# Optimization experiments

Hardware: AMD Instinct MI355X
Metric: run time of the kernel (lower is better)

The kernel has to match this reference:

```python
import jax, jax.numpy as jnp
import numpy as np

HID = 64      # hidden_dim
HEADS = 4     # attention heads
CH = HID // HEADS  # 16 per-head channels
EDIM = 6      # edge_dim
NEG = 0.2     # leaky_relu negative slope


def _glorot(key, shape):
    fan_in, fan_out = shape[0], shape[-1]
    s = np.sqrt(6.0 / (fan_in + fan_out)).astype(np.float32)
    return jax.random.uniform(key, shape, jnp.float32, -s, s)


def setup_inputs() -> dict:
    key = jax.random.key(0)
    ks = iter(jax.random.split(key, 48))
    N, E, T = 100000, 1200000, 20000
    inp = {
        "x": jax.random.normal(next(ks), (N, 7), jnp.float32),
        "pos": jax.random.normal(next(ks), (N, 3), jnp.float32),
        "node_type": jax.random.randint(next(ks), (N,), 0, 2),
        "edge_index": jax.random.randint(next(ks), (2, E), 0, N),
        "edge_attr": jax.random.normal(next(ks), (E, EDIM), jnp.float32),
        "num_tracks": T,
        "hidden_state": jax.random.normal(next(ks), (T, HID), jnp.float32),
        # params
        "type_emb": jax.random.normal(next(ks), (2, 8), jnp.float32),
        "enc_W1": _glorot(next(ks), (18, HID)), "enc_b1": jnp.zeros((HID,), jnp.float32),
        "enc_W2": _glorot(next(ks), (HID, HID)), "enc_b2": jnp.zeros((HID,), jnp.float32),
        "gru_Wi": _glorot(next(ks), (HID, 3 * HID)), "gru_bi": jnp.zeros((3 * HID,), jnp.float32),
        "gru_Wh": _glorot(next(ks), (HID, 3 * HID)), "gru_bh": jnp.zeros((3 * HID,), jnp.float32),
        "dec_W1": _glorot(next(ks), (HID, HID)), "dec_b1": jnp.zeros((HID,), jnp.float32),
        "dec_W2": _glorot(next(ks), (HID, 7)), "dec_b2": jnp.zeros((7,), jnp.float32),
    }
    for g in ("g1", "g2"):
        inp[g + "_Wl"] = _glorot(next(ks), (HID, HID))
        inp[g + "_bl"] = jnp.zeros((HID,), jnp.float32)
        inp[g + "_Wr"] = _glorot(next(ks), (HID, HID))
        inp[g + "_br"] = jnp.zeros((HID,), jnp.float32)
        inp[g + "_We"] = _glorot(next(ks), (EDIM, HID))
        inp[g + "_att"] = _glorot(next(ks), (HEADS, CH))
        inp[g + "_bias"] = jnp.zeros((HID,), jnp.float32)
    return inp


def _segment_softmax(e, seg, n):
    m = jax.ops.segment_max(e, seg, num_segments=n)
    m = jnp.where(jnp.isfinite(m), m, 0.0)
    ex = jnp.exp(e - m[seg])
    s = jax.ops.segment_sum(ex, seg, num_segments=n)
    return ex / (s[seg] + 1e-16)


def _gatv2(h, src, dst, eattr, Wl, bl, Wr, br, We, att, bias):
    N = h.shape[0]
    xl = (h @ Wl + bl).reshape(N, HEADS, CH)
    xr = (h @ Wr + br).reshape(N, HEADS, CH)
    ea = (eattr @ We).reshape(-1, HEADS, CH)
    g = jax.nn.leaky_relu(xl[src] + xr[dst] + ea, NEG)      # [E, H, C]
    e = jnp.einsum('ehc,hc->eh', g, att)                     # [E, H]
    alpha = _segment_softmax(e, dst, N)                      # [E, H]
    msg = xl[src] * alpha[..., None]                         # [E, H, C]
    out = jax.ops.segment_sum(msg, dst, num_segments=N)
    return out.reshape(N, HID) + bias, alpha


def reference(x, pos, node_type, edge_index, edge_attr, num_tracks, hidden_state,
              type_emb, enc_W1, enc_b1, enc_W2, enc_b2,
              g1_Wl, g1_bl, g1_Wr, g1_br, g1_We, g1_att, g1_bias,
              g2_Wl, g2_bl, g2_Wr, g2_br, g2_We, g2_att, g2_bias,
              gru_Wi, gru_bi, gru_Wh, gru_bh,
              dec_W1, dec_b1, dec_W2, dec_b2):
    N = x.shape[0]
    h = jnp.concatenate([x, pos, type_emb[node_type]], axis=-1)
    h = jax.nn.relu(h @ enc_W1 + enc_b1) @ enc_W2 + enc_b2

    # PyG GATv2Conv: add self loops, edge_attr fill_value='mean' (mean of incoming edges)
    src, dst = edge_index[0], edge_index[1]
    deg = jax.ops.segment_sum(jnp.ones(src.shape[0], jnp.float32), dst, num_segments=N)
    loop_attr = jax.ops.segment_sum(edge_attr, dst, num_segments=N) / jnp.maximum(deg, 1.0)[:, None]
    ar = jnp.arange(N)
    src_a = jnp.concatenate([src, ar])
    dst_a = jnp.concatenate([dst, ar])
    eattr_a = jnp.concatenate([edge_attr, loop_attr], axis=0)

    h1, a1 = _gatv2(h, src_a, dst_a, eattr_a, g1_Wl, g1_bl, g1_Wr, g1_br, g1_We, g1_att, g1_bias)
    h1 = jax.nn.relu(h1)
    h2, a2 = _gatv2(h1, src_a, dst_a, eattr_a, g2_Wl, g2_bl, g2_Wr, g2_br, g2_We, g2_att, g2_bias)

    # GRUCell on the first num_tracks nodes
    ht = h2[:num_tracks]
    gi = ht @ gru_Wi + gru_bi
    gh = hidden_state @ gru_Wh + gru_bh
    r = jax.nn.sigmoid(gi[:, :HID] + gh[:, :HID])
    z = jax.nn.sigmoid(gi[:, HID:2 * HID] + gh[:, HID:2 * HID])
    n = jnp.tanh(gi[:, 2 * HID:] + r * gh[:, 2 * HID:])
    new_tracks = (1.0 - z) * n + z * hidden_state

    new_full = jnp.concatenate([new_tracks, h2[num_tracks:]], axis=0)
    out = jax.nn.relu(new_full @ dec_W1 + dec_b1) @ dec_W2 + dec_b2  # [N, 7]
    final = out.at[:, :3].set(pos + out[:, :3])
    final = final.at[:, 3:6].set(x[:, :3] + out[:, 3:6])
    return final, new_full, a1, a2
```

## Files before the change

### kernel.cpp

```cpp
#include <hip/hip_runtime.h>

#define NEG 0.2f
#define LOG2E 1.44269504088896f
typedef unsigned short u16;

__device__ __forceinline__ float sigmoidf_(float v){ return 1.f/(1.f+__expf(-v)); }
__device__ __forceinline__ int rfl_(int v){ return __builtin_amdgcn_readfirstlane(v); }
__device__ __forceinline__ float bf2f_(unsigned u){ return __uint_as_float(u<<16); }
__device__ __forceinline__ u16 f2bf_(float f){
  unsigned u = __float_as_uint(f);
  u += 0x7FFFu + ((u>>16)&1u);
  return (u16)(u>>16);
}
template<int C>
__device__ __forceinline__ float dppadd_(float p){
  int r = __builtin_amdgcn_update_dpp(0, __float_as_int(p), C, 0xF, 0xF, true);
  return p + __int_as_float(r);
}
__device__ __forceinline__ float dppsum16_(float p){
  p = dppadd_<0x121>(p);
  p = dppadd_<0x122>(p);
  p = dppadd_<0x124>(p);
  p = dppadd_<0x128>(p);
  return p;
}

__global__ __launch_bounds__(256) void encdeg_kernel(
    const float* __restrict__ x, const float* __restrict__ pos,
    const int* __restrict__ ntype, const float* __restrict__ temb,
    const float* __restrict__ W1, const float* __restrict__ b1,
    const float* __restrict__ W2, const float* __restrict__ b2,
    float* __restrict__ hout,
    const int* __restrict__ ei, int* __restrict__ deg,
    int encB, int E, int N)
{
  __shared__ float sW1[18*64];
  __shared__ float sW2[4096];
  __shared__ float fT[4][8*20];
  __shared__ float tT[4][8*64];
  if ((int)blockIdx.x >= encB){
    int base = ((int)blockIdx.x - encB)*1024 + (int)threadIdx.x;
    #pragma unroll
    for (int j=0;j<4;j++){
      int e = base + j*256;
      if (e < E) atomicAdd(deg + ei[E+e], 1);
    }
    return;
  }
  for (int i=threadIdx.x; i<18*64; i+=256) sW1[i]=W1[i];
  for (int i=threadIdx.x; i<4096; i+=256)  sW2[i]=W2[i];
  __syncthreads();
  int lane = threadIdx.x & 63;
  int wid  = threadIdx.x >> 6;
  int n0 = (blockIdx.x*4 + wid)*8;
  if (n0 >= N) return;
  float b1v=b1[lane], b2v=b2[lane];
  #pragma unroll
  for (int m=0;m<8;m++){
    int n=n0+m; float fv=0.f;
    if (n<N){
      if (lane<7)       fv=x[(size_t)n*7+lane];
      else if (lane<10) fv=pos[(size_t)n*3+lane-7];
      else if (lane<18) fv=temb[ntype[n]*8+lane-10];
    }
    if (lane<20) fT[wid][m*20+lane]=fv;
  }
  float t[8];
  #pragma unroll
  for (int m=0;m<8;m++) t[m]=b1v;
  #pragma unroll 2
  for (int k=0;k<18;k++){
    float w=sW1[k*64+lane];
    #pragma unroll
    for (int m=0;m<8;m++) t[m] += fT[wid][m*20+k]*w;
  }
  #pragma unroll
  for (int m=0;m<8;m++){ t[m]=fmaxf(t[m],0.f); tT[wid][m*64+lane]=t[m]; }
  float o[8];
  #pragma unroll
  for (int m=0;m<8;m++) o[m]=b2v;
  #pragma unroll 2
  for (int k=0;k<64;k++){
    float w=sW2[k*64+lane];
    #pragma unroll
    for (int m=0;m<8;m++) o[m] += tT[wid][m*64+k]*w;
  }
  #pragma unroll
  for (int m=0;m<8;m++){ int n=n0+m; if (n<N) hout[(size_t)n*64+lane]=o[m]; }
}

__global__ __launch_bounds__(256) void alloc_kernel(
    const int* __restrict__ deg, int* __restrict__ offs, int* __restrict__ cursor,
    int* __restrict__ counter, int N)
{
  __shared__ int wsum[4], woff[4], sbase;
  int lane = threadIdx.x & 63, w = threadIdx.x >> 6;
  int base = blockIdx.x*1024 + threadIdx.x*4;
  int v[4]; int s=0;
  #pragma unroll
  for (int j=0;j<4;j++){ int i=base+j; v[j]=(i<N)?deg[i]:0; s+=v[j]; }
  int inc=s;
  #pragma unroll
  for (int d=1;d<64;d<<=1){ int t=__shfl_up(inc,d); if (lane>=d) inc+=t; }
  if (lane==63) wsum[w]=inc;
  __syncthreads();
  if (threadIdx.x==0){
    woff[0]=0; woff[1]=wsum[0]; woff[2]=wsum[0]+wsum[1]; woff[3]=wsum[0]+wsum[1]+wsum[2];
    sbase = atomicAdd(counter, woff[3]+wsum[3]);
  }
  __syncthreads();
  int excl = sbase + woff[w] + (inc - s);
  #pragma unroll
  for (int j=0;j<4;j++){
    int i=base+j;
    if (i<N){ offs[i]=excl; cursor[i]=excl; }
    excl+=v[j];
  }
}

__global__ __launch_bounds__(256) void xfrmfill_kernel(
    const float* __restrict__ hin,
    const float* __restrict__ Wl, const float* __restrict__ bl,
    const float* __restrict__ Wr, const float* __restrict__ br,
    u16* __restrict__ xlo, u16* __restrict__ xro,
    const int* __restrict__ ei, const float* __restrict__ eattr,
    int* __restrict__ cursor, float4* __restrict__ slots,
    int xfB, int E, int N)
{
  __shared__ float hT[4][16*64];
  if ((int)blockIdx.x >= xfB){
    int base = ((int)blockIdx.x - xfB)*1024 + (int)threadIdx.x;
    #pragma unroll
    for (int j=0;j<4;j++){
      int e = base + j*256;
      if (e < E){
        int dst = ei[E + e];
        unsigned slot = (unsigned)atomicAdd(cursor + dst, 1);
        const float2* ep = (const float2*)(eattr + (size_t)e*6);
        float2 p0=ep[0], p1=ep[1], p2=ep[2];
        float4 a, b;
        a.x = __int_as_float(e); a.y = __int_as_float(ei[e]);
        a.z = p0.x; a.w = p0.y;
        b.x = p1.x; b.y = p1.y; b.z = p2.x; b.w = p2.y;
        slots[slot*2u]   = a;
        slots[slot*2u+1] = b;
      }
    }
    return;
  }
  int lane=threadIdx.x&63;
  int wid=threadIdx.x>>6;
  int n0=(blockIdx.x*4+wid)*16;
  if (n0>=N) return;
  #pragma unroll
  for (int m=0;m<16;m++){
    int n=n0+m;
    hT[wid][m*64+lane] = (n<N)? hin[(size_t)n*64+lane] : 0.f;
  }
  float blv=bl[lane], brv=br[lane];
  float al[16], ar[16];
  #pragma unroll
  for (int m=0;m<16;m++){ al[m]=blv; ar[m]=brv; }
  #pragma unroll 2
  for (int k=0;k<64;k++){
    float wl=Wl[k*64+lane], wr=Wr[k*64+lane];
    #pragma unroll
    for (int m=0;m<16;m++){
      float hb = hT[wid][m*64+k];
      al[m]+=hb*wl; ar[m]+=hb*wr;
    }
  }
  #pragma unroll
  for (int m=0;m<16;m++){
    int n=n0+m;
    if (n<N){ xlo[(((unsigned)n)<<6)+lane]=f2bf_(al[m]); xro[(((unsigned)n)<<6)+lane]=f2bf_(ar[m]); }
  }
}

__global__ __launch_bounds__(256) void xfrm_kernel(
    const float* __restrict__ hin,
    const float* __restrict__ Wl, const float* __restrict__ bl,
    const float* __restrict__ Wr, const float* __restrict__ br,
    u16* __restrict__ xlo, u16* __restrict__ xro, int N)
{
  __shared__ float sWl[4096], sWr[4096];
  __shared__ float hT[4][16*64];
  for (int i=threadIdx.x;i<4096;i+=256){ sWl[i]=Wl[i]; sWr[i]=Wr[i]; }
  __syncthreads();
  int lane=threadIdx.x&63;
  int wid=threadIdx.x>>6;
  int n0=(blockIdx.x*4+wid)*16;
  if (n0>=N) return;
  #pragma unroll
  for (int m=0;m<16;m++){
    int n=n0+m;
    hT[wid][m*64+lane] = (n<N)? hin[(size_t)n*64+lane] : 0.f;
  }
  float blv=bl[lane], brv=br[lane];
  float al[16], ar[16];
  #pragma unroll
  for (int m=0;m<16;m++){ al[m]=blv; ar[m]=brv; }
  #pragma unroll 2
  for (int k=0;k<64;k++){
    float wl=sWl[k*64+lane], wr=sWr[k*64+lane];
    #pragma unroll
    for (int m=0;m<16;m++){
      float hb = hT[wid][m*64+k];
      al[m]+=hb*wl; ar[m]+=hb*wr;
    }
  }
  #pragma unroll
  for (int m=0;m<16;m++){
    int n=n0+m;
    if (n<N){ xlo[(((unsigned)n)<<6)+lane]=f2bf_(al[m]); xro[(((unsigned)n)<<6)+lane]=f2bf_(ar[m]); }
  }
}

#define EDGE_STEP(EIDX, EADD, XV) do {                                       \
    float s_ = (XV) + xrv + (EADD);                                          \
    s_ = fmaxf(s_, NEG*s_);                                                  \
    float p_ = dppsum16_(s_*attv);                                           \
    if (isbase) aout[(((unsigned)(EIDX))<<2)+h] = p_;                        \
    if (__all(p_ <= mmax)) {                                                 \
      float w_ = exp2f(p_ - mmax);                                           \
      ssum += w_; acc += w_*(XV);                                            \
    } else {                                                                 \
      float mn_ = fmaxf(mmax, p_);                                           \
      float sc_ = exp2f(mmax - mn_);                                         \
      float w_  = exp2f(p_ - mn_);                                           \
      ssum = ssum*sc_ + w_;                                                  \
      acc  = acc*sc_ + w_*(XV);                                              \
      mmax = mn_;                                                            \
    }                                                                        \
  } while(0)

#define EDGE_PRE(J, OO) \
    float4 u##J = slots[(unsigned)(OO)*2u], v##J = slots[(unsigned)(OO)*2u+1u]; \
    int e##J = rfl_(__float_as_int(u##J.x)); \
    int s##J = rfl_(__float_as_int(u##J.y)); \
    unsigned xv##J = xlb[(((unsigned)s##J)<<6)+lane];

#define EDGE_BODY(J) \
    float d##J = u##J.z*we0 + u##J.w*we1 + v##J.x*we2 + v##J.y*we3 + v##J.z*we4 + v##J.w*we5; \
    dsum += d##J; \
    EDGE_STEP(e##J, d##J, bf2f_(xv##J));

__global__ __launch_bounds__(256) void gat_kernel(
    const float4* __restrict__ slots, const int* __restrict__ offs, const int* __restrict__ deg,
    const u16* __restrict__ xlb, const u16* __restrict__ xrb,
    const float* __restrict__ We, const float* __restrict__ att,
    const float* __restrict__ bias,
    float* __restrict__ aout, float2* __restrict__ msbuf,
    float* __restrict__ hout,
    int E, int N, int do_relu)
{
  int lane = threadIdx.x & 63;
  int n = blockIdx.x*4 + (threadIdx.x>>6);
  if (n >= N) return;
  float we0=We[lane], we1=We[64+lane], we2=We[128+lane],
        we3=We[192+lane], we4=We[256+lane], we5=We[320+lane];
  float attv = att[lane] * LOG2E;
  float bv = bias[lane];
  float xrv = bf2f_(xrb[(((unsigned)n)<<6)+lane]);
  int h = lane >> 4;
  bool isbase = (lane & 15) == 0;
  int o0 = rfl_(offs[n]);
  int dg = rfl_(deg[n]);
  int oend = o0 + dg;
  float mmax = -3.402823e38f, ssum=0.f, acc=0.f, dsum=0.f;
  int o = o0;
  for (; o+4 <= oend; o += 4){
    EDGE_PRE(0,o); EDGE_PRE(1,o+1); EDGE_PRE(2,o+2); EDGE_PRE(3,o+3);
    EDGE_BODY(0); EDGE_BODY(1); EDGE_BODY(2); EDGE_BODY(3);
  }
  for (; o < oend; ++o){
    EDGE_PRE(0,o);
    EDGE_BODY(0);
  }
  {
    float dS = dsum * (1.f/fmaxf((float)dg,1.f));
    float xvS = bf2f_((unsigned)xlb[(((unsigned)n)<<6)+lane]);
    EDGE_STEP(E+n, dS, xvS);
  }
  float sinv = 1.f/(ssum + 1e-16f);
  if (isbase) msbuf[(((unsigned)n)<<2)+h] = make_float2(mmax, sinv);
  float outv = acc*sinv + bv;
  if (do_relu) outv = fmaxf(outv, 0.f);
  hout[(((unsigned)n)<<6)+lane] = outv;
}

__global__ __launch_bounds__(256) void grudecalpha_kernel(
    const float* __restrict__ h2, const float* __restrict__ hid,
    const float* __restrict__ Wi, const float* __restrict__ bi,
    const float* __restrict__ Wh, const float* __restrict__ bh,
    const int* __restrict__ Tptr,
    const float* __restrict__ W1, const float* __restrict__ b1,
    const float* __restrict__ W2, const float* __restrict__ b2,
    const float* __restrict__ x, const float* __restrict__ pos,
    float* __restrict__ nf, float* __restrict__ fout,
    const int* __restrict__ ei,
    const float2* __restrict__ ms1, const float2* __restrict__ ms2,
    float4* __restrict__ a1, float4* __restrict__ a2,
    int gdB, int E, int N)
{
  __shared__ float sW2[448];
  __shared__ float sb2[8];
  __shared__ float tT[4][8*68];
  __shared__ float pT[4][8*68];
  if ((int)blockIdx.x >= gdB){
    int e = ((int)blockIdx.x - gdB)*256 + (int)threadIdx.x;
    if (e < E+N){
      int dst = (e<E)? ei[E+e] : (e-E);
      {
        float4 r = a1[e];
        const float2* mp = ms1 + (((unsigned)dst)<<2);
        float2 m0=mp[0], m1=mp[1], m2=mp[2], m3=mp[3];
        float4 o;
        o.x = exp2f(r.x - m0.x)*m0.y;
        o.y = exp2f(r.y - m1.x)*m1.y;
        o.z = exp2f(r.z - m2.x)*m2.y;
        o.w = exp2f(r.w - m3.x)*m3.y;
        a1[e] = o;
      }
      {
        float4 r = a2[e];
        const float2* mp = ms2 + (((unsigned)dst)<<2);
        float2 m0=mp[0], m1=mp[1], m2=mp[2], m3=mp[3];
        float4 o;
        o.x = exp2f(r.x - m0.x)*m0.y;
        o.y = exp2f(r.y - m1.x)*m1.y;
        o.z = exp2f(r.z - m2.x)*m2.y;
        o.w = exp2f(r.w - m3.x)*m3.y;
        a2[e] = o;
      }
    }
    return;
  }
  for (int i=threadIdx.x;i<448;i+=256) sW2[i]=W2[i];
  if (threadIdx.x<7)  sb2[threadIdx.x]=b2[threadIdx.x];
  __syncthreads();
  int lane = threadIdx.x & 63;
  int wid  = threadIdx.x >> 6;
  int n0 = (blockIdx.x*4 + wid)*8;
  if (n0 >= N) return;
  int T = *Tptr;
  float hv[8], nfv[8];
  #pragma unroll
  for (int m=0;m<8;m++){ int n=n0+m; hv[m] = (n<N)? h2[(size_t)n*64+lane] : 0.f; }
  if (n0 < T){
    float pv[8];
    #pragma unroll
    for (int m=0;m<8;m++){ int n=n0+m; pv[m] = (n<T)? hid[(size_t)n*64+lane] : 0.f; }
    #pragma unroll
    for (int m=0;m<8;m++){ tT[wid][m*68+lane]=hv[m]; pT[wid][m*68+lane]=pv[m]; }
    float gr[8],gz[8],gn[8],hr[8],hz[8],hn[8];
    #pragma unroll
    for (int m=0;m<8;m++){ gr[m]=0.f;gz[m]=0.f;gn[m]=0.f;hr[m]=0.f;hz[m]=0.f;hn[m]=0.f; }
    for (int k=0;k<64;k++){
      float wir=Wi[k*192+lane], wiz=Wi[k*192+64+lane], win=Wi[k*192+128+lane];
      float whr=Wh[k*192+lane], whz=Wh[k*192+64+lane], whn=Wh[k*192+128+lane];
      #pragma unroll
      for (int m=0;m<8;m++){
        float a=tT[wid][m*68+k], b=pT[wid][m*68+k];
        gr[m]+=a*wir; gz[m]+=a*wiz; gn[m]+=a*win;
        hr[m]+=b*whr; hz[m]+=b*whz; hn[m]+=b*whn;
      }
    }
    float bir=bi[lane], biz=bi[64+lane], bin=bi[128+lane];
    float bhr=bh[lane], bhz=bh[64+lane], bhn=bh[128+lane];
    #pragma unroll
    for (int m=0;m<8;m++){
      int n=n0+m;
      if (n<T){
        float r  = sigmoidf_(gr[m]+bir + hr[m]+bhr);
        float z  = sigmoidf_(gz[m]+biz + hz[m]+bhz);
        float nn = tanhf(gn[m]+bin + r*(hn[m]+bhn));
        nfv[m] = (1.f-z)*nn + z*pv[m];
      } else {
        nfv[m] = hv[m];
      }
    }
  } else {
    #pragma unroll
    for (int m=0;m<8;m++) nfv[m] = hv[m];
  }
  #pragma unroll
  for (int m=0;m<8;m++){ int n=n0+m; if (n<N) nf[(size_t)n*64+lane]=nfv[m]; }
  #pragma unroll
  for (int m=0;m<8;m++) tT[wid][m*68+lane]=nfv[m];
  float t[8];
  float b1v=b1[lane];
  #pragma unroll
  for (int m=0;m<8;m++) t[m]=b1v;
  #pragma unroll 2
  for (int k=0;k<64;k++){
    float w=W1[k*64+lane];
    #pragma unroll
    for (int m=0;m<8;m++) t[m] += tT[wid][m*68+k]*w;
  }
  #pragma unroll
  for (int m=0;m<8;m++) t[m]=fmaxf(t[m],0.f);
  #pragma unroll
  for (int m=0;m<8;m++) tT[wid][m*68+lane]=t[m];
  int mm = lane >> 3, cc = lane & 7;
  if (cc < 7){
    float a2v = sb2[cc];
    #pragma unroll 4
    for (int k=0;k<64;k++) a2v += tT[wid][mm*68+k]*sW2[k*7+cc];
    int n = n0+mm;
    if (n < N){
      if (cc<3)      a2v += pos[(size_t)n*3+cc];
      else if (cc<6) a2v += x[(size_t)n*7+(cc-3)];
      fout[(size_t)n*7+cc] = a2v;
    }
  }
}

extern "C" void kernel_launch(void* const* d_in, const int* in_sizes, int n_in,
                              void* d_out, int out_size, void* d_ws, size_t ws_size,
                              hipStream_t stream)
{
  const float* x     = (const float*)d_in[0];
  const float* pos   = (const float*)d_in[1];
  const int*   ntype = (const int*)d_in[2];
  const int*   eidx  = (const int*)d_in[3];
  const float* eattr = (const float*)d_in[4];
  const int*   Tptr  = (const int*)d_in[5];
  const float* hid   = (const float*)d_in[6];
  const float* temb  = (const float*)d_in[7];
  const float* encW1 = (const float*)d_in[8];
  const float* encb1 = (const float*)d_in[9];
  const float* encW2 = (const float*)d_in[10];
  const float* encb2 = (const float*)d_in[11];
  const float* gruWi = (const float*)d_in[12];
  const float* grubi = (const float*)d_in[13];
  const float* gruWh = (const float*)d_in[14];
  const float* grubh = (const float*)d_in[15];
  const float* decW1 = (const float*)d_in[16];
  const float* decb1 = (const float*)d_in[17];
  const float* decW2 = (const float*)d_in[18];
  const float* decb2 = (const float*)d_in[19];
  const float* gWl[2]  = {(const float*)d_in[20], (const float*)d_in[27]};
  const float* gbl[2]  = {(const float*)d_in[21], (const float*)d_in[28]};
  const float* gWr[2]  = {(const float*)d_in[22], (const float*)d_in[29]};
  const float* gbr[2]  = {(const float*)d_in[23], (const float*)d_in[30]};
  const float* gWe[2]  = {(const float*)d_in[24], (const float*)d_in[31]};
  const float* gatt[2] = {(const float*)d_in[25], (const float*)d_in[32]};
  const float* gbias[2]= {(const float*)d_in[26], (const float*)d_in[33]};

  int N  = in_sizes[0] / 7;
  int E  = in_sizes[3] / 2;
  int Ea = E + N;

  char* w = (char*)d_ws;
  float* A      = (float*)w; w += (size_t)N*64*sizeof(float);
  u16*   XL     = (u16*)w;  w += (size_t)N*64*sizeof(u16);
  u16*   XR     = (u16*)w;  w += (size_t)N*64*sizeof(u16);
  float2* msbuf1= (float2*)w; w += (size_t)N*4*sizeof(float2);
  float2* msbuf2= (float2*)w; w += (size_t)N*4*sizeof(float2);
  float4* slots = (float4*)w; w += (size_t)E*32;
  int*   deg    = (int*)w;   w += (size_t)N*sizeof(int);
  int*   counter= (int*)w;   w += 4*sizeof(int);
  int*   cursor = (int*)w;   w += (size_t)N*sizeof(int);
  int*   offs   = (int*)w;   w += (size_t)N*sizeof(int);

  float* out_final = (float*)d_out;
  float* out_nf    = out_final + (size_t)N*7;
  float* out_a1    = out_nf + (size_t)N*64;
  float* out_a2    = out_a1 + (size_t)Ea*4;

  hipMemsetAsync(deg, 0, ((size_t)N + 4)*sizeof(int), stream);

  int encB = (N+31)/32;
  int degB = (E+1023)/1024;
  encdeg_kernel<<<encB+degB, 256, 0, stream>>>(x,pos,ntype,temb,encW1,encb1,encW2,encb2,A,
      eidx, deg, encB, E, N);

  alloc_kernel<<<(N+1023)/1024, 256, 0, stream>>>(deg, offs, cursor, counter, N);

  int xfB = (N+63)/64;
  int flB = (E+1023)/1024;
  xfrmfill_kernel<<<xfB+flB, 256, 0, stream>>>(A, gWl[0], gbl[0], gWr[0], gbr[0], XL, XR,
      eidx, eattr, cursor, slots, xfB, E, N);

  int gatB = (N+3)/4;
  gat_kernel<<<gatB, 256, 0, stream>>>(slots, offs, deg, XL, XR,
      gWe[0], gatt[0], gbias[0], out_a1, msbuf1, A, E, N, 1);

  xfrm_kernel<<<xfB, 256, 0, stream>>>(A, gWl[1], gbl[1], gWr[1], gbr[1], XL, XR, N);

  gat_kernel<<<gatB, 256, 0, stream>>>(slots, offs, deg, XL, XR,
      gWe[1], gatt[1], gbias[1], out_a2, msbuf2, A, E, N, 0);

  int gdB = (N+31)/32;
  int alB = (Ea+255)/256;
  grudecalpha_kernel<<<gdB+alB, 256, 0, stream>>>(A, hid, gruWi, grubi, gruWh, grubh, Tptr,
      decW1, decb1, decW2, decb2, x, pos, out_nf, out_final,
      eidx, msbuf1, msbuf2, (float4*)out_a1, (float4*)out_a2, gdB, E, N);
}
```

Baseline: 515.5 us.

## Fuse encoder into first GAT transform and normalize attention in-place inside GAT kernel

Moves the node encoder MLP into the first linear-transform/fill kernel so the encoded features stay in shared memory instead of going through global memory. The degree-counting part becomes its own kernel. The separate alpha normalization pass, which read per-node max/sum buffers, is replaced by a second loop inside each GAT kernel that rereads the slot edge ids and rescales that node's raw scores in place. This removes the max/sum buffers and one full pass over the alpha arrays. In exchange it adds scattered read-modify-write traffic inside the GAT kernels and puts the encoder's extra compute on the path before the fill.

```diff
diff --git a/kernel.cpp b/kernel.cpp
--- a/kernel.cpp
+++ b/kernel.cpp
@@ -25,68 +25,14 @@
   return p;
 }
 
-__global__ __launch_bounds__(256) void encdeg_kernel(
-    const float* __restrict__ x, const float* __restrict__ pos,
-    const int* __restrict__ ntype, const float* __restrict__ temb,
-    const float* __restrict__ W1, const float* __restrict__ b1,
-    const float* __restrict__ W2, const float* __restrict__ b2,
-    float* __restrict__ hout,
-    const int* __restrict__ ei, int* __restrict__ deg,
-    int encB, int E, int N)
-{
-  __shared__ float sW1[18*64];
-  __shared__ float sW2[4096];
-  __shared__ float fT[4][8*20];
-  __shared__ float tT[4][8*64];
-  if ((int)blockIdx.x >= encB){
-    int base = ((int)blockIdx.x - encB)*1024 + (int)threadIdx.x;
-    #pragma unroll
-    for (int j=0;j<4;j++){
-      int e = base + j*256;
-      if (e < E) atomicAdd(deg + ei[E+e], 1);
-    }
-    return;
-  }
-  for (int i=threadIdx.x; i<18*64; i+=256) sW1[i]=W1[i];
-  for (int i=threadIdx.x; i<4096; i+=256)  sW2[i]=W2[i];
-  __syncthreads();
-  int lane = threadIdx.x & 63;
-  int wid  = threadIdx.x >> 6;
-  int n0 = (blockIdx.x*4 + wid)*8;
-  if (n0 >= N) return;
-  float b1v=b1[lane], b2v=b2[lane];
-  #pragma unroll
-  for (int m=0;m<8;m++){
-    int n=n0+m; float fv=0.f;
-    if (n<N){
-      if (lane<7)       fv=x[(size_t)n*7+lane];
-      else if (lane<10) fv=pos[(size_t)n*3+lane-7];
-      else if (lane<18) fv=temb[ntype[n]*8+lane-10];
-    }
-    if (lane<20) fT[wid][m*20+lane]=fv;
-  }
-  float t[8];
-  #pragma unroll
-  for (int m=0;m<8;m++) t[m]=b1v;
-  #pragma unroll 2
-  for (int k=0;k<18;k++){
-    float w=sW1[k*64+lane];
-    #pragma unroll
-    for (int m=0;m<8;m++) t[m] += fT[wid][m*20+k]*w;
-  }
-  #pragma unroll
-  for (int m=0;m<8;m++){ t[m]=fmaxf(t[m],0.f); tT[wid][m*64+lane]=t[m]; }
-  float o[8];
-  #pragma unroll
-  for (int m=0;m<8;m++) o[m]=b2v;
-  #pragma unroll 2
-  for (int k=0;k<64;k++){
-    float w=sW2[k*64+lane];
-    #pragma unroll
-    for (int m=0;m<8;m++) o[m] += tT[wid][m*64+k]*w;
-  }
-  #pragma unroll
-  for (int m=0;m<8;m++){ int n=n0+m; if (n<N) hout[(size_t)n*64+lane]=o[m]; }
+__global__ void deg_kernel(const int* __restrict__ ei, int* __restrict__ deg, int E)
+{
+  int base = blockIdx.x*1024 + threadIdx.x;
+  #pragma unroll
+  for (int j=0;j<4;j++){
+    int e = base + j*256;
+    if (e < E) atomicAdd(deg + ei[E+e], 1);
+  }
 }
 
 __global__ __launch_bounds__(256) void alloc_kernel(
@@ -118,18 +64,22 @@
   }
 }
 
-__global__ __launch_bounds__(256) void xfrmfill_kernel(
-    const float* __restrict__ hin,
+__global__ __launch_bounds__(256) void encxfill_kernel(
+    const float* __restrict__ x, const float* __restrict__ pos,
+    const int* __restrict__ ntype, const float* __restrict__ temb,
+    const float* __restrict__ eW1, const float* __restrict__ eb1,
+    const float* __restrict__ eW2, const float* __restrict__ eb2,
     const float* __restrict__ Wl, const float* __restrict__ bl,
     const float* __restrict__ Wr, const float* __restrict__ br,
     u16* __restrict__ xlo, u16* __restrict__ xro,
     const int* __restrict__ ei, const float* __restrict__ eattr,
     int* __restrict__ cursor, float4* __restrict__ slots,
-    int xfB, int E, int N)
-{
-  __shared__ float hT[4][16*64];
-  if ((int)blockIdx.x >= xfB){
-    int base = ((int)blockIdx.x - xfB)*1024 + (int)threadIdx.x;
+    int exB, int E, int N)
+{
+  __shared__ float fT[4][8*20];
+  __shared__ float tT[4][8*64];
+  if ((int)blockIdx.x >= exB){
+    int base = ((int)blockIdx.x - exB)*1024 + (int)threadIdx.x;
     #pragma unroll
     for (int j=0;j<4;j++){
       int e = base + j*256;
@@ -148,30 +98,59 @@
     }
     return;
   }
-  int lane=threadIdx.x&63;
-  int wid=threadIdx.x>>6;
-  int n0=(blockIdx.x*4+wid)*16;
-  if (n0>=N) return;
-  #pragma unroll
-  for (int m=0;m<16;m++){
-    int n=n0+m;
-    hT[wid][m*64+lane] = (n<N)? hin[(size_t)n*64+lane] : 0.f;
-  }
+  int lane = threadIdx.x & 63;
+  int wid  = threadIdx.x >> 6;
+  int n0 = (blockIdx.x*4 + wid)*8;
+  if (n0 >= N) return;
+  #pragma unroll
+  for (int m=0;m<8;m++){
+    int n=n0+m; float fv=0.f;
+    if (n<N){
+      if (lane<7)       fv=x[(size_t)n*7+lane];
+      else if (lane<10) fv=pos[(size_t)n*3+lane-7];
+      else if (lane<18) fv=temb[ntype[n]*8+lane-10];
+    }
+    if (lane<20) fT[wid][m*20+lane]=fv;
+  }
+  float t[8];
+  float b1v=eb1[lane];
+  #pragma unroll
+  for (int m=0;m<8;m++) t[m]=b1v;
+  #pragma unroll 2
+  for (int k=0;k<18;k++){
+    float w=eW1[k*64+lane];
+    #pragma unroll
+    for (int m=0;m<8;m++) t[m] += fT[wid][m*20+k]*w;
+  }
+  #pragma unroll
+  for (int m=0;m<8;m++){ t[m]=fmaxf(t[m],0.f); tT[wid][m*64+lane]=t[m]; }
+  float o[8];
+  float b2v=eb2[lane];
+  #pragma unroll
+  for (int m=0;m<8;m++) o[m]=b2v;
+  #pragma unroll 2
+  for (int k=0;k<64;k++){
+    float w=eW2[k*64+lane];
+    #pragma unroll
+    for (int m=0;m<8;m++) o[m] += tT[wid][m*64+k]*w;
+  }
+  #pragma unroll
+  for (int m=0;m<8;m++) tT[wid][m*64+lane]=o[m];
   float blv=bl[lane], brv=br[lane];
-  float al[16], ar[16];
-  #pragma unroll
-  for (int m=0;m<16;m++){ al[m]=blv; ar[m]=brv; }
+  float al[8], ar[8];
+  #pragma unroll
+  for (int m=0;m<8;m++){ al[m]=blv; ar[m]=brv; }
   #pragma unroll 2
   for (int k=0;k<64;k++){
     float wl=Wl[k*64+lane], wr=Wr[k*64+lane];
     #pragma unroll
-    for (int m=0;m<16;m++){
-      float hb = hT[wid][m*64+k];
+    for (int m=0;m<8;m++){
+      float hb = tT[wid][m*64+k];
       al[m]+=hb*wl; ar[m]+=hb*wr;
     }
   }
   #pragma unroll
-  for (int m=0;m<16;m++){
+  for (int m=0;m<8;m++){
     int n=n0+m;
     if (n<N){ xlo[(((unsigned)n)<<6)+lane]=f2bf_(al[m]); xro[(((unsigned)n)<<6)+lane]=f2bf_(ar[m]); }
   }
@@ -221,6 +200,7 @@
     s_ = fmaxf(s_, NEG*s_);                                                  \
     float p_ = dppsum16_(s_*attv);                                           \
     if (isbase) aout[(((unsigned)(EIDX))<<2)+h] = p_;                        \
+    lastp = p_;                                                              \
     if (__all(p_ <= mmax)) {                                                 \
       float w_ = exp2f(p_ - mmax);                                           \
       ssum += w_; acc += w_*(XV);                                            \
@@ -250,8 +230,7 @@
     const u16* __restrict__ xlb, const u16* __restrict__ xrb,
     const float* __restrict__ We, const float* __restrict__ att,
     const float* __restrict__ bias,
-    float* __restrict__ aout, float2* __restrict__ msbuf,
-    float* __restrict__ hout,
+    float* __restrict__ aout, float* __restrict__ hout,
     int E, int N, int do_relu)
 {
   int lane = threadIdx.x & 63;
@@ -267,7 +246,7 @@
   int o0 = rfl_(offs[n]);
   int dg = rfl_(deg[n]);
   int oend = o0 + dg;
-  float mmax = -3.402823e38f, ssum=0.f, acc=0.f, dsum=0.f;
+  float mmax = -3.402823e38f, ssum=0.f, acc=0.f, dsum=0.f, lastp=0.f;
   int o = o0;
   for (; o+4 <= oend; o += 4){
     EDGE_PRE(0,o); EDGE_PRE(1,o+1); EDGE_PRE(2,o+2); EDGE_PRE(3,o+3);
@@ -283,13 +262,35 @@
     EDGE_STEP(E+n, dS, xvS);
   }
   float sinv = 1.f/(ssum + 1e-16f);
-  if (isbase) msbuf[(((unsigned)n)<<2)+h] = make_float2(mmax, sinv);
+  asm volatile("s_waitcnt vmcnt(0)" ::: "memory");
+  o = o0;
+  for (; o+4 <= oend; o += 4){
+    int e0 = __float_as_int(slots[(unsigned)o*2u].x);
+    int e1 = __float_as_int(slots[(unsigned)(o+1)*2u].x);
+    int e2 = __float_as_int(slots[(unsigned)(o+2)*2u].x);
+    int e3 = __float_as_int(slots[(unsigned)(o+3)*2u].x);
+    if (isbase){
+      unsigned i0=(((unsigned)e0)<<2)+h, i1=(((unsigned)e1)<<2)+h,
+               i2=(((unsigned)e2)<<2)+h, i3=(((unsigned)e3)<<2)+h;
+      float r0=aout[i0], r1=aout[i1], r2=aout[i2], r3=aout[i3];
+      aout[i0]=exp2f(r0-mmax)*sinv; aout[i1]=exp2f(r1-mmax)*sinv;
+      aout[i2]=exp2f(r2-mmax)*sinv; aout[i3]=exp2f(r3-mmax)*sinv;
+    }
+  }
+  for (; o < oend; ++o){
+    int e0 = __float_as_int(slots[(unsigned)o*2u].x);
+    if (isbase){
+      unsigned i0=(((unsigned)e0)<<2)+h;
+      aout[i0]=exp2f(aout[i0]-mmax)*sinv;
+    }
+  }
+  if (isbase) aout[(((unsigned)(E+n))<<2)+h] = exp2f(lastp-mmax)*sinv;
   float outv = acc*sinv + bv;
   if (do_relu) outv = fmaxf(outv, 0.f);
   hout[(((unsigned)n)<<6)+lane] = outv;
 }
 
-__global__ __launch_bounds__(256) void grudecalpha_kernel(
+__global__ __launch_bounds__(256) void grudec_kernel(
     const float* __restrict__ h2, const float* __restrict__ hid,
     const float* __restrict__ Wi, const float* __restrict__ bi,
     const float* __restrict__ Wh, const float* __restrict__ bh,
@@ -297,45 +298,12 @@
     const float* __restrict__ W1, const float* __restrict__ b1,
     const float* __restrict__ W2, const float* __restrict__ b2,
     const float* __restrict__ x, const float* __restrict__ pos,
-    float* __restrict__ nf, float* __restrict__ fout,
-    const int* __restrict__ ei,
-    const float2* __restrict__ ms1, const float2* __restrict__ ms2,
-    float4* __restrict__ a1, float4* __restrict__ a2,
-    int gdB, int E, int N)
+    float* __restrict__ nf, float* __restrict__ fout, int N)
 {
   __shared__ float sW2[448];
   __shared__ float sb2[8];
   __shared__ float tT[4][8*68];
   __shared__ float pT[4][8*68];
-  if ((int)blockIdx.x >= gdB){
-    int e = ((int)blockIdx.x - gdB)*256 + (int)threadIdx.x;
-    if (e < E+N){
-      int dst = (e<E)? ei[E+e] : (e-E);
-      {
-        float4 r = a1[e];
-        const float2* mp = ms1 + (((unsigned)dst)<<2);
-        float2 m0=mp[0], m1=mp[1], m2=mp[2], m3=mp[3];
-        float4 o;
-        o.x = exp2f(r.x - m0.x)*m0.y;
-        o.y = exp2f(r.y - m1.x)*m1.y;
-        o.z = exp2f(r.z - m2.x)*m2.y;
-        o.w = exp2f(r.w - m3.x)*m3.y;
-        a1[e] = o;
-      }
-      {
-        float4 r = a2[e];
-        const float2* mp = ms2 + (((unsigned)dst)<<2);
-        float2 m0=mp[0], m1=mp[1], m2=mp[2], m3=mp[3];
-        float4 o;
-        o.x = exp2f(r.x - m0.x)*m0.y;
-        o.y = exp2f(r.y - m1.x)*m1.y;
-        o.z = exp2f(r.z - m2.x)*m2.y;
-        o.w = exp2f(r.w - m3.x)*m3.y;
-        a2[e] = o;
-      }
-    }
-    return;
-  }
   for (int i=threadIdx.x;i<448;i+=256) sW2[i]=W2[i];
   if (threadIdx.x<7)  sb2[threadIdx.x]=b2[threadIdx.x];
   __syncthreads();
@@ -456,8 +424,6 @@
   float* A      = (float*)w; w += (size_t)N*64*sizeof(float);
   u16*   XL     = (u16*)w;  w += (size_t)N*64*sizeof(u16);
   u16*   XR     = (u16*)w;  w += (size_t)N*64*sizeof(u16);
-  float2* msbuf1= (float2*)w; w += (size_t)N*4*sizeof(float2);
-  float2* msbuf2= (float2*)w; w += (size_t)N*4*sizeof(float2);
   float4* slots = (float4*)w; w += (size_t)E*32;
   int*   deg    = (int*)w;   w += (size_t)N*sizeof(int);
   int*   counter= (int*)w;   w += 4*sizeof(int);
@@ -471,30 +437,25 @@
 
   hipMemsetAsync(deg, 0, ((size_t)N + 4)*sizeof(int), stream);
 
-  int encB = (N+31)/32;
-  int degB = (E+1023)/1024;
-  encdeg_kernel<<<encB+degB, 256, 0, stream>>>(x,pos,ntype,temb,encW1,encb1,encW2,encb2,A,
-      eidx, deg, encB, E, N);
-
+  deg_kernel<<<(E+1023)/1024, 256, 0, stream>>>(eidx, deg, E);
   alloc_kernel<<<(N+1023)/1024, 256, 0, stream>>>(deg, offs, cursor, counter, N);
 
-  int xfB = (N+63)/64;
+  int exB = (N+31)/32;
   int flB = (E+1023)/1024;
-  xfrmfill_kernel<<<xfB+flB, 256, 0, stream>>>(A, gWl[0], gbl[0], gWr[0], gbr[0], XL, XR,
-      eidx, eattr, cursor, slots, xfB, E, N);
+  encxfill_kernel<<<exB+flB, 256, 0, stream>>>(x, pos, ntype, temb,
+      encW1, encb1, encW2, encb2, gWl[0], gbl[0], gWr[0], gbr[0], XL, XR,
+      eidx, eattr, cursor, slots, exB, E, N);
 
   int gatB = (N+3)/4;
   gat_kernel<<<gatB, 256, 0, stream>>>(slots, offs, deg, XL, XR,
-      gWe[0], gatt[0], gbias[0], out_a1, msbuf1, A, E, N, 1);
-
+      gWe[0], gatt[0], gbias[0], out_a1, A, E, N, 1);
+
+  int xfB = (N+63)/64;
   xfrm_kernel<<<xfB, 256, 0, stream>>>(A, gWl[1], gbl[1], gWr[1], gbr[1], XL, XR, N);
 
   gat_kernel<<<gatB, 256, 0, stream>>>(slots, offs, deg, XL, XR,
-      gWe[1], gatt[1], gbias[1], out_a2, msbuf2, A, E, N, 0);
-
-  int gdB = (N+31)/32;
-  int alB = (Ea+255)/256;
-  grudecalpha_kernel<<<gdB+alB, 256, 0, stream>>>(A, hid, gruWi, grubi, gruWh, grubh, Tptr,
-      decW1, decb1, decW2, decb2, x, pos, out_nf, out_final,
-      eidx, msbuf1, msbuf2, (float4*)out_a1, (float4*)out_a2, gdB, E, N);
-}
+      gWe[1], gatt[1], gbias[1], out_a2, A, E, N, 0);
+
+  grudec_kernel<<<(N+31)/32, 256, 0, stream>>>(A, hid, gruWi, grubi, gruWh, grubh, Tptr,
+      decW1, decb1, decW2, decb2, x, pos, out_nf, out_final, N);
+}
```

Result: slower. 541.6 us (+5.1%).
